# Performance work log

Measured on AMD Instinct MI355X. Metric: run time of the kernel, lower is better.

The kernel has to match this reference:

```python
import jax, jax.numpy as jnp
import numpy as np

B, C, H, W = 8, 64, 64, 64
CQ = C // 2

def setup_inputs() -> dict:
    key = jax.random.key(0)
    ks = jax.random.split(key, 10)
    s = 0.05
    return {
        "x": jax.random.normal(ks[0], (B, C, H, W), jnp.float32),
        "wq": jax.random.normal(ks[1], (CQ, C), jnp.float32) * s,
        "bq": jax.random.normal(ks[2], (CQ,), jnp.float32) * s,
        "wk": jax.random.normal(ks[3], (CQ, C), jnp.float32) * s,
        "bk": jax.random.normal(ks[4], (CQ,), jnp.float32) * s,
        "wv": jax.random.normal(ks[5], (C, C), jnp.float32) * s,
        "bv": jax.random.normal(ks[6], (C,), jnp.float32) * s,
        "wf": jax.random.normal(ks[7], (C, C), jnp.float32) * s,
        "bf": jax.random.normal(ks[8], (C,), jnp.float32) * s,
        "gamma": jnp.ones((1,), jnp.float32),
    }

def _conv1x1(w, b, x):
    # 1x1 conv == channel matmul: [O,C] x [B,C,H,W] -> [B,O,H,W]
    return jnp.einsum('oc,bchw->bohw', w, x) + b[None, :, None, None]

def reference(x, wq, bq, wk, bk, wv, bv, wf, bf, gamma):
    b, c, h, w = x.shape
    n = h * w
    q = _conv1x1(wq, bq, x).reshape(b, -1, n)   # [B, C/2, N]
    k = _conv1x1(wk, bk, x).reshape(b, -1, n)   # [B, C/2, N]
    v = _conv1x1(wv, bv, x).reshape(b, c, n)    # [B, C,   N]
    scale = 1.0 / jnp.sqrt(jnp.float32(n))
    energy = jnp.einsum('bcn,bcm->bnm', q, k) * scale  # [B, N, N]
    attn = jax.nn.softmax(energy, axis=-1)
    out = jnp.einsum('bcm,bnm->bcn', v, attn)          # V @ attn^T
    out = out.reshape(b, c, h, w)
    out = _conv1x1(wf, bf, out)
    return gamma[0] * out + x
```

## Files before the change

### kernel.cpp

```cpp
#include <hip/hip_runtime.h>

typedef unsigned short u16;
typedef unsigned int   u32;
typedef __bf16  bf16x8 __attribute__((ext_vector_type(8)));
typedef float   f32x16 __attribute__((ext_vector_type(16)));
typedef u32     u32x4  __attribute__((ext_vector_type(4)));

#define NN  4096
#define CCH 64
#define CQ  32
#define K1S 0.0225421092623961f

__device__ __forceinline__ u16 bfc(float a) { return __builtin_bit_cast(u16, (__bf16)a); }

__device__ __forceinline__ u32 e2pk(float a, float b) {
  float ea, eb; u32 r;
  asm("v_exp_f32 %0, %1" : "=v"(ea) : "v"(a));
  asm("v_exp_f32 %0, %1" : "=v"(eb) : "v"(b));
  asm("v_cvt_pk_bf16_f32 %0, %1, %2" : "=v"(r) : "v"(ea), "v"(eb));
  return r;
}

__device__ __forceinline__ void gload16(const void* g, void* l) {
  __builtin_amdgcn_global_load_lds((const __attribute__((address_space(1))) void*)g,
                                   (__attribute__((address_space(3))) void*)l, 16, 0, 0);
}


__global__ __launch_bounds__(512) void qkv_kernel(
    const float* __restrict__ x,
    const float* __restrict__ wq, const float* __restrict__ bq,
    const float* __restrict__ wk, const float* __restrict__ bk,
    const float* __restrict__ wv, const float* __restrict__ bv,
    u16* __restrict__ qT, char* __restrict__ kws, char* __restrict__ vws)
{
  __shared__ u16 qls[64][34];
  __shared__ u16 kls[64][34];
  __shared__ u16 vls[64][66];
  const int bid = blockIdx.x;
  const int b = bid >> 6;
  const int chunk = bid & 63;
  const int nbase = chunk * 64;
  const int t = threadIdx.x, lane = t & 63, wid = t >> 6;

  const float* xb = x + (size_t)b * CCH * NN + nbase + lane;
  float xcol[64];
  #pragma unroll
  for (int c = 0; c < 64; ++c) xcol[c] = xb[(size_t)c * NN];

  const float* w; const float* bias; float sc = 1.0f;
  const int sub = (wid & 1) * 16;
  if (wid < 2)      { w = wq + sub * 64; bias = bq + sub; sc = K1S; }
  else if (wid < 4) { w = wk + sub * 64; bias = bk + sub; }
  else              { w = wv + (wid - 4) * 16 * 64; bias = bv + (wid - 4) * 16; }

  for (int i = 0; i < 16; ++i) {
    float a = bias[i];
    #pragma unroll
    for (int c = 0; c < 64; ++c) a = fmaf(w[i * 64 + c], xcol[c], a);
    a *= sc;
    u16 hv = bfc(a);
    if (wid < 2)      qls[lane][sub + i] = hv;
    else if (wid < 4) kls[lane][sub + i] = hv;
    else              vls[(wid - 4) * 16 + i][lane] = hv;
  }
  __syncthreads();

  u32* qdst = (u32*)(qT + ((size_t)b * NN + nbase) * CQ);
  #pragma unroll
  for (int jj = 0; jj < 2; ++jj) {
    int i = t + 512 * jj;
    int n = i >> 4, cp = i & 15;
    qdst[i] = *(const u32*)&qls[n][cp * 2];
  }
  u32* kimg = (u32*)(kws + ((size_t)b * 64 + chunk) * 4096);
  #pragma unroll
  for (int jj = 0; jj < 2; ++jj) {
    int i = t + 512 * jj;
    int reg = i >> 8, l = (i >> 2) & 63, j2 = i & 3;
    int s = reg >> 1, ks = reg & 1;
    int key = s * 32 + (l & 31);
    int ck  = ks * 16 + (l >> 5) * 8 + j2 * 2;
    kimg[i] = *(const u32*)&kls[key][ck];
  }
  u32* vimg = (u32*)(vws + ((size_t)b * 64 + chunk) * 8192);
  #pragma unroll
  for (int jj = 0; jj < 4; ++jj) {
    int i = t + 512 * jj;
    int reg = i >> 8, l = (i >> 2) & 63, j2 = i & 3;
    int s = reg >> 2, kb = (reg >> 1) & 1, ct = reg & 1;
    int c   = ct * 32 + (l & 31);
    int key = s * 32 + kb * 16 + (l >> 5) * 4 + (j2 >> 1) * 8 + (j2 & 1) * 2;
    vimg[i] = *(const u32*)&vls[c][key];
  }
}

template<int NSPLIT>
__global__ __launch_bounds__(256, 2) void attn_kernel(
    const u16* __restrict__ qT, const char* __restrict__ kws, const char* __restrict__ vws,
    u32* __restrict__ opart, float* __restrict__ lpart)
{
  constexpr int CH = 64 / NSPLIT;
  __shared__ __align__(16) char kbuf[2][4096];
  __shared__ __align__(16) char vbuf[2][8192];
  const int bid = blockIdx.x;
  const int b = bid & 7, qt = (bid >> 3) & 15, split = bid >> 7;
  const int t = threadIdx.x, lane = t & 63, wid = t >> 6;
  const int h = lane >> 5, c31 = lane & 31;

  const u16* qpA = qT + ((size_t)b * NN + qt * 256 + wid * 64 + c31) * CQ + h * 8;
  const bf16x8 qfA0 = *(const bf16x8*)(qpA);
  const bf16x8 qfA1 = *(const bf16x8*)(qpA + 16);
  const bf16x8 qfB0 = *(const bf16x8*)(qpA + 32 * CQ);
  const bf16x8 qfB1 = *(const bf16x8*)(qpA + 32 * CQ + 16);

  const char* ksrc = kws + ((size_t)b * 64 + split * CH) * 4096 + t * 16;
  const char* vsrc = vws + ((size_t)b * 64 + split * CH) * 8192 + t * 16;

  auto stage = [&](int cur, int it) {
    gload16(ksrc + (size_t)it * 4096, &kbuf[cur][wid * 1024]);
    gload16(vsrc + (size_t)it * 8192, &vbuf[cur][wid * 1024]);
    gload16(vsrc + (size_t)it * 8192 + 4096, &vbuf[cur][4096 + wid * 1024]);
  };

  const bf16x8 onef = __builtin_bit_cast(bf16x8,
      (u32x4){0x3F803F80u, 0x3F803F80u, 0x3F803F80u, 0x3F803F80u});

  f32x16 accA0 = {}, accA1 = {}, accB0 = {}, accB1 = {}, laccA = {}, laccB = {};
  const int lofs = lane * 16;

  stage(0, 0);
  __syncthreads();

  auto body = [&](int cur, int it) {
    if (it < CH - 1) stage(cur ^ 1, it + 1);

    const bf16x8 kf0 = *(const bf16x8*)&kbuf[cur][lofs];
    const bf16x8 kf1 = *(const bf16x8*)&kbuf[cur][1024 + lofs];
    const bf16x8 kf2 = *(const bf16x8*)&kbuf[cur][2048 + lofs];
    const bf16x8 kf3 = *(const bf16x8*)&kbuf[cur][3072 + lofs];

    f32x16 sA0, sA1, sB0, sB1;
    sA0 = __builtin_amdgcn_mfma_f32_32x32x16_bf16(kf0, qfA0, (f32x16){}, 0, 0, 0);
    sA0 = __builtin_amdgcn_mfma_f32_32x32x16_bf16(kf1, qfA1, sA0, 0, 0, 0);
    sA1 = __builtin_amdgcn_mfma_f32_32x32x16_bf16(kf2, qfA0, (f32x16){}, 0, 0, 0);
    sA1 = __builtin_amdgcn_mfma_f32_32x32x16_bf16(kf3, qfA1, sA1, 0, 0, 0);
    sB0 = __builtin_amdgcn_mfma_f32_32x32x16_bf16(kf0, qfB0, (f32x16){}, 0, 0, 0);
    sB0 = __builtin_amdgcn_mfma_f32_32x32x16_bf16(kf1, qfB1, sB0, 0, 0, 0);
    sB1 = __builtin_amdgcn_mfma_f32_32x32x16_bf16(kf2, qfB0, (f32x16){}, 0, 0, 0);
    sB1 = __builtin_amdgcn_mfma_f32_32x32x16_bf16(kf3, qfB1, sB1, 0, 0, 0);

    u32 pwA[16] __attribute__((aligned(16)));
    u32 pwB[16] __attribute__((aligned(16)));
    #pragma unroll
    for (int r = 0; r < 16; r += 2) {
      pwA[r >> 1]       = e2pk(sA0[r], sA0[r + 1]);
      pwA[8 + (r >> 1)] = e2pk(sA1[r], sA1[r + 1]);
      pwB[r >> 1]       = e2pk(sB0[r], sB0[r + 1]);
      pwB[8 + (r >> 1)] = e2pk(sB1[r], sB1[r + 1]);
    }

    #pragma unroll
    for (int s = 0; s < 2; ++s) {
      #pragma unroll
      for (int kb = 0; kb < 2; ++kb) {
        const bf16x8 pfA = __builtin_bit_cast(bf16x8, *(const u32x4*)&pwA[s * 8 + kb * 4]);
        const bf16x8 pfB = __builtin_bit_cast(bf16x8, *(const u32x4*)&pwB[s * 8 + kb * 4]);
        const bf16x8 vf0 = *(const bf16x8*)&vbuf[cur][(s * 4 + kb * 2) * 1024 + lofs];
        const bf16x8 vf1 = *(const bf16x8*)&vbuf[cur][(s * 4 + kb * 2 + 1) * 1024 + lofs];
        accA0 = __builtin_amdgcn_mfma_f32_32x32x16_bf16(vf0, pfA, accA0, 0, 0, 0);
        accA1 = __builtin_amdgcn_mfma_f32_32x32x16_bf16(vf1, pfA, accA1, 0, 0, 0);
        accB0 = __builtin_amdgcn_mfma_f32_32x32x16_bf16(vf0, pfB, accB0, 0, 0, 0);
        accB1 = __builtin_amdgcn_mfma_f32_32x32x16_bf16(vf1, pfB, accB1, 0, 0, 0);
        laccA = __builtin_amdgcn_mfma_f32_32x32x16_bf16(onef, pfA, laccA, 0, 0, 0);
        laccB = __builtin_amdgcn_mfma_f32_32x32x16_bf16(onef, pfB, laccB, 0, 0, 0);
      }
    }
    __syncthreads();
  };

  for (int i2 = 0; i2 < CH / 2; ++i2) { body(0, 2 * i2); body(1, 2 * i2 + 1); }

  const int qt128 = qt * 2 + (wid >> 1);
  const size_t obase = ((size_t)(b * 32 + qt128) * NSPLIT + split) * 4096;
  #pragma unroll
  for (int j = 0; j < 2; ++j) {
    const int col = (wid & 1) * 64 + j * 32 + c31;
    #pragma unroll
    for (int ct = 0; ct < 2; ++ct) {
      const f32x16& a = j ? (ct ? accB1 : accB0) : (ct ? accA1 : accA0);
      #pragma unroll
      for (int g2 = 0; g2 < 4; ++g2) {
        #pragma unroll
        for (int b2 = 0; b2 < 2; ++b2) {
          int cp = ct * 16 + g2 * 4 + h * 2 + b2;
          float lo = a[g2 * 4 + b2 * 2], hi = a[g2 * 4 + b2 * 2 + 1];
          u32 pr; asm("v_cvt_pk_bf16_f32 %0, %1, %2" : "=v"(pr) : "v"(lo), "v"(hi));
          opart[obase + cp * 128 + col] = pr;
        }
      }
    }
    if (h == 0) {
      const f32x16& l = j ? laccB : laccA;
      lpart[((size_t)(b * 32 + qt128) * NSPLIT + split) * 128 + col] = l[0];
    }
  }
}

template<int NSPLIT>
__global__ __launch_bounds__(256) void combine_kernel(
    const u32* __restrict__ opart, const float* __restrict__ lpart,
    const float* __restrict__ x, const float* __restrict__ wf, const float* __restrict__ bfb,
    const float* __restrict__ gamma, float* __restrict__ out)
{
  __shared__ float ols[64][65];
  __shared__ float linv[64];
  const int bid = blockIdx.x;
  const int b = bid & 7, qt64 = bid >> 3;
  const int qt128 = qt64 >> 1, qh = qt64 & 1;
  const int t = threadIdx.x;

  const u32* ob = opart + (size_t)(b * 32 + qt128) * NSPLIT * 4096 + qh * 64;
  #pragma unroll
  for (int jj = 0; jj < 8; ++jj) {
    int i = t + 256 * jj;
    int cp = i >> 6, q = i & 63;
    float lo = 0.f, hi = 0.f;
    #pragma unroll
    for (int s = 0; s < NSPLIT; ++s) {
      u32 a = ob[s * 4096 + cp * 128 + q];
      lo += __builtin_bit_cast(float, (a << 16));
      hi += __builtin_bit_cast(float, (a & 0xffff0000u));
    }
    ols[cp * 2][q]     = lo;
    ols[cp * 2 + 1][q] = hi;
  }
  if (t < 64) {
    const float* lp = lpart + (size_t)(b * 32 + qt128) * NSPLIT * 128 + qh * 64;
    float l = 0.f;
    #pragma unroll
    for (int s = 0; s < NSPLIT; ++s) l += lp[s * 128 + t];
    linv[t] = 1.f / l;
  }
  __syncthreads();

  const int q = t & 63, og = t >> 6;
  const float oinv = linv[q];
  float oc[64];
  #pragma unroll
  for (int c = 0; c < 64; ++c) oc[c] = ols[c][q] * oinv;
  const float gm = gamma[0];
  const size_t nidx = (size_t)qt64 * 64 + q;
  for (int i = 0; i < 16; ++i) {
    const int o = og * 16 + i;
    float a = bfb[o];
    #pragma unroll
    for (int c = 0; c < 64; ++c) a = fmaf(wf[o * 64 + c], oc[c], a);
    const size_t idx = ((size_t)b * CCH + o) * NN + nidx;
    out[idx] = gm * a + x[idx];
  }
}

extern "C" void kernel_launch(void* const* d_in, const int* in_sizes, int n_in,
                              void* d_out, int out_size, void* d_ws, size_t ws_size,
                              hipStream_t stream) {
  const float* x     = (const float*)d_in[0];
  const float* wq    = (const float*)d_in[1];
  const float* bq    = (const float*)d_in[2];
  const float* wk    = (const float*)d_in[3];
  const float* bk    = (const float*)d_in[4];
  const float* wv    = (const float*)d_in[5];
  const float* bv    = (const float*)d_in[6];
  const float* wf    = (const float*)d_in[7];
  const float* bf_   = (const float*)d_in[8];
  const float* gamma = (const float*)d_in[9];
  float* out = (float*)d_out;

  u16* qT   = (u16*)d_ws;
  char* kws = (char*)(qT + (size_t)8 * NN * CQ);
  char* vws = kws + (size_t)8 * 64 * 4096;
  u32* opart = (u32*)(vws + (size_t)8 * 64 * 8192);
  const size_t base = 2097152ull + 2097152ull + 4194304ull;
  const size_t need8 = base + 8ull * (4194304ull + 131072ull);
  const size_t need4 = base + 4ull * (4194304ull + 131072ull);

  qkv_kernel<<<dim3(512), dim3(512), 0, stream>>>(x, wq, bq, wk, bk, wv, bv, qT, kws, vws);
  if (ws_size >= need8) {
    float* lpart = (float*)(opart + (size_t)8 * 32 * 8 * 4096);
    attn_kernel<8><<<dim3(1024), dim3(256), 0, stream>>>(qT, kws, vws, opart, lpart);
    combine_kernel<8><<<dim3(512), dim3(256), 0, stream>>>(opart, lpart, x, wf, bf_, gamma, out);
  } else if (ws_size >= need4) {
    float* lpart = (float*)(opart + (size_t)8 * 32 * 4 * 4096);
    attn_kernel<4><<<dim3(512), dim3(256), 0, stream>>>(qT, kws, vws, opart, lpart);
    combine_kernel<4><<<dim3(512), dim3(256), 0, stream>>>(opart, lpart, x, wf, bf_, gamma, out);
  } else {
    float* lpart = (float*)(opart + (size_t)8 * 32 * 2 * 4096);
    attn_kernel<2><<<dim3(256), dim3(256), 0, stream>>>(qT, kws, vws, opart, lpart);
    combine_kernel<2><<<dim3(512), dim3(256), 0, stream>>>(opart, lpart, x, wf, bf_, gamma, out);
  }
}
```

Before: 98.23 us.

## Triple-buffer attention K/V loads with vmcnt waits; widen combine kernel

The attention kernel moves from a double-buffered LDS ring with __syncthreads to a three-stage ring that prefetches two iterations ahead. It replaces full syncs with explicit s_waitcnt vmcnt plus s_barrier, and raises wave priority around the MFMA blocks. The combine kernel now runs 512 threads per block, so each wave computes 8 output channels instead of 16. This is meant to hide global-to-LDS latency and shorten the epilogue, at the cost of more LDS (36KB per block), which may lower occupancy, and of relying on hand-tuned vmcnt counts.

```diff
diff --git a/kernel.cpp b/kernel.cpp
--- a/kernel.cpp
+++ b/kernel.cpp
@@ -101,8 +101,8 @@
     u32* __restrict__ opart, float* __restrict__ lpart)
 {
   constexpr int CH = 64 / NSPLIT;
-  __shared__ __align__(16) char kbuf[2][4096];
-  __shared__ __align__(16) char vbuf[2][8192];
+  __shared__ __align__(16) char kbuf[3][4096];
+  __shared__ __align__(16) char vbuf[3][8192];
   const int bid = blockIdx.x;
   const int b = bid & 7, qt = (bid >> 3) & 15, split = bid >> 7;
   const int t = threadIdx.x, lane = t & 63, wid = t >> 6;
@@ -117,10 +117,10 @@
   const char* ksrc = kws + ((size_t)b * 64 + split * CH) * 4096 + t * 16;
   const char* vsrc = vws + ((size_t)b * 64 + split * CH) * 8192 + t * 16;
 
-  auto stage = [&](int cur, int it) {
-    gload16(ksrc + (size_t)it * 4096, &kbuf[cur][wid * 1024]);
-    gload16(vsrc + (size_t)it * 8192, &vbuf[cur][wid * 1024]);
-    gload16(vsrc + (size_t)it * 8192 + 4096, &vbuf[cur][4096 + wid * 1024]);
+  auto stage = [&](int buf, int it) {
+    gload16(ksrc + (size_t)it * 4096, &kbuf[buf][wid * 1024]);
+    gload16(vsrc + (size_t)it * 8192, &vbuf[buf][wid * 1024]);
+    gload16(vsrc + (size_t)it * 8192 + 4096, &vbuf[buf][4096 + wid * 1024]);
   };
 
   const bf16x8 onef = __builtin_bit_cast(bf16x8,
@@ -130,10 +130,16 @@
   const int lofs = lane * 16;
 
   stage(0, 0);
-  __syncthreads();
-
-  auto body = [&](int cur, int it) {
-    if (it < CH - 1) stage(cur ^ 1, it + 1);
+  stage(1, 1);
+
+  #pragma unroll
+  for (int it = 0; it < CH; ++it) {
+    if (it == CH - 1) asm volatile("s_waitcnt vmcnt(0)" ::: "memory");
+    else              asm volatile("s_waitcnt vmcnt(3)" ::: "memory");
+    __builtin_amdgcn_s_barrier();
+    __builtin_amdgcn_sched_barrier(0);
+    if (it + 2 < CH) stage((it + 2) % 3, it + 2);
+    const int cur = it % 3;
 
     const bf16x8 kf0 = *(const bf16x8*)&kbuf[cur][lofs];
     const bf16x8 kf1 = *(const bf16x8*)&kbuf[cur][1024 + lofs];
@@ -141,6 +147,7 @@
     const bf16x8 kf3 = *(const bf16x8*)&kbuf[cur][3072 + lofs];
 
     f32x16 sA0, sA1, sB0, sB1;
+    __builtin_amdgcn_s_setprio(1);
     sA0 = __builtin_amdgcn_mfma_f32_32x32x16_bf16(kf0, qfA0, (f32x16){}, 0, 0, 0);
     sA0 = __builtin_amdgcn_mfma_f32_32x32x16_bf16(kf1, qfA1, sA0, 0, 0, 0);
     sA1 = __builtin_amdgcn_mfma_f32_32x32x16_bf16(kf2, qfA0, (f32x16){}, 0, 0, 0);
@@ -149,6 +156,7 @@
     sB0 = __builtin_amdgcn_mfma_f32_32x32x16_bf16(kf1, qfB1, sB0, 0, 0, 0);
     sB1 = __builtin_amdgcn_mfma_f32_32x32x16_bf16(kf2, qfB0, (f32x16){}, 0, 0, 0);
     sB1 = __builtin_amdgcn_mfma_f32_32x32x16_bf16(kf3, qfB1, sB1, 0, 0, 0);
+    __builtin_amdgcn_s_setprio(0);
 
     u32 pwA[16] __attribute__((aligned(16)));
     u32 pwB[16] __attribute__((aligned(16)));
@@ -160,6 +168,7 @@
       pwB[8 + (r >> 1)] = e2pk(sB1[r], sB1[r + 1]);
     }
 
+    __builtin_amdgcn_s_setprio(1);
     #pragma unroll
     for (int s = 0; s < 2; ++s) {
       #pragma unroll
@@ -176,10 +185,8 @@
         laccB = __builtin_amdgcn_mfma_f32_32x32x16_bf16(onef, pfB, laccB, 0, 0, 0);
       }
     }
-    __syncthreads();
-  };
-
-  for (int i2 = 0; i2 < CH / 2; ++i2) { body(0, 2 * i2); body(1, 2 * i2 + 1); }
+    __builtin_amdgcn_s_setprio(0);
+  }
 
   const int qt128 = qt * 2 + (wid >> 1);
   const size_t obase = ((size_t)(b * 32 + qt128) * NSPLIT + split) * 4096;
@@ -208,7 +215,7 @@
 }
 
 template<int NSPLIT>
-__global__ __launch_bounds__(256) void combine_kernel(
+__global__ __launch_bounds__(512) void combine_kernel(
     const u32* __restrict__ opart, const float* __restrict__ lpart,
     const float* __restrict__ x, const float* __restrict__ wf, const float* __restrict__ bfb,
     const float* __restrict__ gamma, float* __restrict__ out)
@@ -218,12 +225,12 @@
   const int bid = blockIdx.x;
   const int b = bid & 7, qt64 = bid >> 3;
   const int qt128 = qt64 >> 1, qh = qt64 & 1;
-  const int t = threadIdx.x;
+  const int t = threadIdx.x, lane = t & 63, wid = t >> 6;
 
   const u32* ob = opart + (size_t)(b * 32 + qt128) * NSPLIT * 4096 + qh * 64;
   #pragma unroll
-  for (int jj = 0; jj < 8; ++jj) {
-    int i = t + 256 * jj;
+  for (int jj = 0; jj < 4; ++jj) {
+    int i = t + 512 * jj;
     int cp = i >> 6, q = i & 63;
     float lo = 0.f, hi = 0.f;
     #pragma unroll
@@ -244,15 +251,15 @@
   }
   __syncthreads();
 
-  const int q = t & 63, og = t >> 6;
-  const float oinv = linv[q];
+  const float oinv = linv[lane];
   float oc[64];
   #pragma unroll
-  for (int c = 0; c < 64; ++c) oc[c] = ols[c][q] * oinv;
+  for (int c = 0; c < 64; ++c) oc[c] = ols[c][lane] * oinv;
   const float gm = gamma[0];
-  const size_t nidx = (size_t)qt64 * 64 + q;
-  for (int i = 0; i < 16; ++i) {
-    const int o = og * 16 + i;
+  const size_t nidx = (size_t)qt64 * 64 + lane;
+  #pragma unroll
+  for (int i = 0; i < 8; ++i) {
+    const int o = wid * 8 + i;
     float a = bfb[o];
     #pragma unroll
     for (int c = 0; c < 64; ++c) a = fmaf(wf[o * 64 + c], oc[c], a);
@@ -288,14 +295,14 @@
   if (ws_size >= need8) {
     float* lpart = (float*)(opart + (size_t)8 * 32 * 8 * 4096);
     attn_kernel<8><<<dim3(1024), dim3(256), 0, stream>>>(qT, kws, vws, opart, lpart);
-    combine_kernel<8><<<dim3(512), dim3(256), 0, stream>>>(opart, lpart, x, wf, bf_, gamma, out);
+    combine_kernel<8><<<dim3(512), dim3(512), 0, stream>>>(opart, lpart, x, wf, bf_, gamma, out);
   } else if (ws_size >= need4) {
     float* lpart = (float*)(opart + (size_t)8 * 32 * 4 * 4096);
     attn_kernel<4><<<dim3(512), dim3(256), 0, stream>>>(qT, kws, vws, opart, lpart);
-    combine_kernel<4><<<dim3(512), dim3(256), 0, stream>>>(opart, lpart, x, wf, bf_, gamma, out);
+    combine_kernel<4><<<dim3(512), dim3(512), 0, stream>>>(opart, lpart, x, wf, bf_, gamma, out);
   } else {
     float* lpart = (float*)(opart + (size_t)8 * 32 * 2 * 4096);
     attn_kernel<2><<<dim3(256), dim3(256), 0, stream>>>(qT, kws, vws, opart, lpart);
-    combine_kernel<2><<<dim3(512), dim3(256), 0, stream>>>(opart, lpart, x, wf, bf_, gamma, out);
-  }
-}
+    combine_kernel<2><<<dim3(512), dim3(512), 0, stream>>>(opart, lpart, x, wf, bf_, gamma, out);
+  }
+}
```

After: 98.41 us. Within noise of the previous version (+0.2%).
